# Performance work log

Measured on AMD Instinct MI355X. Metric: run time of the kernel, lower is better.

Reference implementation:

```python
import jax, jax.numpy as jnp
import numpy as np

N_PROBLEMS = 20000
N_SKILLS = 1000
EMB_SIZE = 128
TIME_LOG = 5.0
B, L = 64, 1024


def setup_inputs() -> dict:
    key = jax.random.key(0)
    ks = jax.random.split(key, 10)
    skills = jax.random.randint(ks[0], (B, L), 0, N_SKILLS)
    problems = jax.random.randint(ks[1], (B, L), 0, N_PROBLEMS)
    labels = jax.random.randint(ks[2], (B, L), 0, 2)
    times = jnp.sort(jax.random.randint(ks[3], (B, L), 0, 1_000_000), axis=-1)
    inp = jnp.stack([skills, problems, labels, times], axis=1)  # [B,4,L]
    std = 0.01
    return {
        "input": inp,
        "problem_base": std * jax.random.normal(ks[4], (N_PROBLEMS, 1), jnp.float32),
        "skill_base": std * jax.random.normal(ks[5], (N_SKILLS, 1), jnp.float32),
        "alpha_inter": std * jax.random.normal(ks[6], (N_SKILLS * 2, EMB_SIZE), jnp.float32),
        "alpha_skill": std * jax.random.normal(ks[7], (N_SKILLS, EMB_SIZE), jnp.float32),
        "beta_inter": std * jax.random.normal(ks[8], (N_SKILLS * 2, EMB_SIZE), jnp.float32),
        "beta_skill": std * jax.random.normal(ks[9], (N_SKILLS, EMB_SIZE), jnp.float32),
    }


def reference(input, problem_base, skill_base, alpha_inter, alpha_skill, beta_inter, beta_skill):
    skills = input[:, 0]    # [B,L]
    problems = input[:, 1]
    labels = input[:, 2]
    times = input[:, 3]

    mask_labels = labels * (labels < 2).astype(labels.dtype)
    inters = skills + mask_labels * N_SKILLS  # [B,L] in [0, 2*N_SKILLS)

    # pairwise Hawkes excitation / decay scores: [B,L,L]
    alphas = jnp.einsum('bie,bje->bij', alpha_inter[inters], alpha_skill[skills])
    betas = jnp.einsum('bie,bje->bij', beta_inter[inters], beta_skill[skills])
    betas = jnp.clip(betas + 1.0, 0.0, 10.0)

    dt = jnp.abs(times[:, :, None] - times[:, None, :]).astype(jnp.float32)
    log_dt = jnp.log(dt + 1e-10) / np.log(TIME_LOG)

    cross_effects = alphas * jnp.exp(-betas * log_dt)

    seq_len = skills.shape[1]
    # keep strictly-upper-triangular entries (source i before target j)
    keep = jnp.triu(jnp.ones((seq_len, seq_len), dtype=bool), k=1)
    sum_t = jnp.where(keep[None], cross_effects, 0.0).sum(axis=-2)  # [B,L]

    problem_bias = problem_base[problems][..., 0]
    skill_bias = skill_base[skills][..., 0]
    return jax.nn.sigmoid(problem_bias + skill_bias + sum_t)
```

## Files before the change

kernel.cpp:

```cpp
#include <hip/hip_runtime.h>
#include <hip/hip_bf16.h>

#define NB   64
#define SL   1024
#define EMB  128
#define NSK  1000
#define NS   4

#define AI_OFF 0
#define BI_OFF 256000
#define AS_OFF 512000
#define BS_OFF 640000
#define TB_ELEMS 768000
#define ACC_BYTE_OFF (TB_ELEMS * 2)

using short8  = __attribute__((ext_vector_type(8))) short;
using floatx4 = __attribute__((ext_vector_type(4))) float;

#define INV_LOG2_5 0.43067655807339306f

__device__ inline unsigned cvt2(float x, float y) {
    float2 f; f.x = x; f.y = y;
    __hip_bfloat162 h = __float22bfloat162_rn(f);
    unsigned u; __builtin_memcpy(&u, &h, sizeof(u));
    return u;
}

extern "C" __global__ __launch_bounds__(256)
void cvt_tables(const float* __restrict__ ai, const float* __restrict__ bi,
                const float* __restrict__ as, const float* __restrict__ bs,
                unsigned short* __restrict__ dst)
{
    const int t = blockIdx.x * 256 + threadIdx.x;
    const long e = (long)t * 8;
    const float* src;
    if      (e < 256000) src = ai + e;
    else if (e < 512000) src = bi + (e - 256000);
    else if (e < 640000) src = as + (e - 512000);
    else                 src = bs + (e - 640000);
    float4 f0 = *(const float4*)src;
    float4 f1 = *(const float4*)(src + 4);
    uint4 pk;
    pk.x = cvt2(f0.x, f0.y); pk.y = cvt2(f0.z, f0.w);
    pk.z = cvt2(f1.x, f1.y); pk.w = cvt2(f1.z, f1.w);
    *(uint4*)(dst + e) = pk;
}

__device__ float fixup_pair(const float* __restrict__ air,
                            const float* __restrict__ bir,
                            const float* __restrict__ asr,
                            const float* __restrict__ bsr) {
    float da = 0.f, db = 0.f;
    for (int k = 0; k < EMB; ++k) {
        da += air[k] * asr[k];
        db += bir[k] * bsr[k];
    }
    float beta = fminf(fmaxf(db + 1.f, 0.f), 10.f);
    return da * __expf(beta * 14.30676558073393f);
}

extern "C" __global__ __launch_bounds__(256, 2)
void hawkes_main(const int*   __restrict__ inp,
                 const unsigned short* __restrict__ tb,
                 float*       __restrict__ acc)
{
    __shared__ unsigned short lA[2][64][128];

    const int bid  = blockIdx.x;
    const int b    = bid & (NB - 1);
    const int r    = bid >> 6;
    const int jt   = 7 - (r >> 2);
    const int s    = r & 3;
    const int tid  = threadIdx.x;
    const int w    = tid >> 6;
    const int l    = tid & 63;
    const int quad = l >> 4;
    const int col  = l & 15;

    const int* __restrict__ binp = inp + b * 4 * SL;

    const int j0 = jt * 128 + w * 16 + col;
    const int j1 = j0 + 64;
    const int sk0 = binp[j0],          sk1 = binp[j1];
    const int tj0 = binp[3 * SL + j0], tj1 = binp[3 * SL + j1];

    short8 bfa0[4], bfb0[4], bfa1[4], bfb1[4];
    {
        const unsigned short* p0a = tb + AS_OFF + (long)sk0 * EMB + quad * 8;
        const unsigned short* p0b = tb + BS_OFF + (long)sk0 * EMB + quad * 8;
        const unsigned short* p1a = tb + AS_OFF + (long)sk1 * EMB + quad * 8;
        const unsigned short* p1b = tb + BS_OFF + (long)sk1 * EMB + quad * 8;
#pragma unroll
        for (int ks = 0; ks < 4; ++ks) {
            bfa0[ks] = *(const short8*)(p0a + ks * 32);
            bfb0[ks] = *(const short8*)(p0b + ks * 32);
            bfa1[ks] = *(const short8*)(p1a + ks * 32);
            bfb1[ks] = *(const short8*)(p1b + ks * 32);
        }
    }

    const int srow = tid >> 2;
    const int sq   = tid & 3;
    const int sw   = srow & 15;
    unsigned short* rowA = &lA[0][srow][0];
    unsigned short* rowB = &lA[1][srow][0];

    float sum0 = 0.f, sum1 = 0.f;
    const int itmax = 2 * jt + 1;

    if (s <= itmax) {
        uint4 pa0, pa1, pa2, pa3, pb0, pb1, pb2, pb3;
        {
            const int irow  = s * 64 + srow;
            const int ski   = binp[irow];
            const int li    = binp[2 * SL + irow];
            const long intr = ski + (long)li * NSK;
            const unsigned short* sA  = tb + AI_OFF + intr * EMB + sq * 32;
            const unsigned short* sBm = tb + BI_OFF + intr * EMB + sq * 32;
            pa0 = *(const uint4*)(sA);      pa1 = *(const uint4*)(sA + 8);
            pa2 = *(const uint4*)(sA + 16); pa3 = *(const uint4*)(sA + 24);
            pb0 = *(const uint4*)(sBm);     pb1 = *(const uint4*)(sBm + 8);
            pb2 = *(const uint4*)(sBm + 16);pb3 = *(const uint4*)(sBm + 24);
        }

        for (int it = s; it <= itmax; it += NS) {
            __syncthreads();
            *(uint4*)(rowA + (((sq * 4 + 0) ^ sw) * 8)) = pa0;
            *(uint4*)(rowA + (((sq * 4 + 1) ^ sw) * 8)) = pa1;
            *(uint4*)(rowA + (((sq * 4 + 2) ^ sw) * 8)) = pa2;
            *(uint4*)(rowA + (((sq * 4 + 3) ^ sw) * 8)) = pa3;
            *(uint4*)(rowB + (((sq * 4 + 0) ^ sw) * 8)) = pb0;
            *(uint4*)(rowB + (((sq * 4 + 1) ^ sw) * 8)) = pb1;
            *(uint4*)(rowB + (((sq * 4 + 2) ^ sw) * 8)) = pb2;
            *(uint4*)(rowB + (((sq * 4 + 3) ^ sw) * 8)) = pb3;

            if (it + NS <= itmax) {
                const int irow  = (it + NS) * 64 + srow;
                const int ski   = binp[irow];
                const int li    = binp[2 * SL + irow];
                const long intr = ski + (long)li * NSK;
                const unsigned short* sA  = tb + AI_OFF + intr * EMB + sq * 32;
                const unsigned short* sBm = tb + BI_OFF + intr * EMB + sq * 32;
                pa0 = *(const uint4*)(sA);      pa1 = *(const uint4*)(sA + 8);
                pa2 = *(const uint4*)(sA + 16); pa3 = *(const uint4*)(sA + 24);
                pb0 = *(const uint4*)(sBm);     pb1 = *(const uint4*)(sBm + 8);
                pb2 = *(const uint4*)(sBm + 16);pb3 = *(const uint4*)(sBm + 24);
            }
            __syncthreads();

            const int itb = it * 64;
#pragma unroll
            for (int isub = 0; isub < 4; ++isub) {
                floatx4 aa0 = {0.f,0.f,0.f,0.f}, bb0 = {0.f,0.f,0.f,0.f};
                floatx4 aa1 = {0.f,0.f,0.f,0.f}, bb1 = {0.f,0.f,0.f,0.f};
                const unsigned short* rrow0 = &lA[0][isub * 16 + col][0];
                const unsigned short* rrow1 = &lA[1][isub * 16 + col][0];
#pragma unroll
                for (int ks = 0; ks < 4; ++ks) {
                    const int pc = ((ks * 4 + quad) ^ col) * 8;
                    short8 av = *(const short8*)(rrow0 + pc);
                    short8 bv = *(const short8*)(rrow1 + pc);
                    aa0 = __builtin_amdgcn_mfma_f32_16x16x32_bf16(av, bfa0[ks], aa0, 0, 0, 0);
                    aa1 = __builtin_amdgcn_mfma_f32_16x16x32_bf16(av, bfa1[ks], aa1, 0, 0, 0);
                    bb0 = __builtin_amdgcn_mfma_f32_16x16x32_bf16(bv, bfb0[ks], bb0, 0, 0, 0);
                    bb1 = __builtin_amdgcn_mfma_f32_16x16x32_bf16(bv, bfb1[ks], bb1, 0, 0, 0);
                }
                const int ibase = itb + isub * 16 + quad * 4;
                const int4 t4 = *(const int4*)(binp + 3 * SL + ibase);
#pragma unroll
                for (int rr = 0; rr < 4; ++rr) {
                    const int ti = (rr == 0) ? t4.x : (rr == 1) ? t4.y : (rr == 2) ? t4.z : t4.w;
                    {
                        const int dt = tj0 - ti;
                        float lc  = __log2f((float)dt);
                        float nb  = fminf(fmaxf(bb0[rr] + 1.f, 0.f), 10.f) * (-INV_LOG2_5);
                        float arg = (dt > 0) ? nb * lc : -__builtin_inff();
                        sum0 += aa0[rr] * exp2f(arg);
                    }
                    {
                        const int dt = tj1 - ti;
                        float lc  = __log2f((float)dt);
                        float nb  = fminf(fmaxf(bb1[rr] + 1.f, 0.f), 10.f) * (-INV_LOG2_5);
                        float arg = (dt > 0) ? nb * lc : -__builtin_inff();
                        sum1 += aa1[rr] * exp2f(arg);
                    }
                }
            }
        }
    }

    sum0 += __shfl_xor(sum0, 16, 64); sum0 += __shfl_xor(sum0, 32, 64);
    sum1 += __shfl_xor(sum1, 16, 64); sum1 += __shfl_xor(sum1, 32, 64);

    if (quad == 0) {
        float* as_ = acc + (((long)s * NB + b) << 10);
        as_[j0] = sum0;
        as_[j1] = sum1;
    }
}

extern "C" __global__ __launch_bounds__(256)
void hawkes_finalize(const int* __restrict__ inp, const float* __restrict__ pbase,
                     const float* __restrict__ sbase,
                     const float* __restrict__ ai, const float* __restrict__ as,
                     const float* __restrict__ bi, const float* __restrict__ bs,
                     const float* __restrict__ acc, float* __restrict__ out)
{
    const int t = blockIdx.x * 256 + threadIdx.x;
    const int b = t >> 10, j = t & (SL - 1);
    const int* binp = inp + b * 4 * SL;
    const int tj   = binp[3 * SL + j];
    const int sk_j = binp[j];

    float corr = 0.f;
    for (int i = j - 1; i >= 0 && binp[3 * SL + i] == tj; --i) {
        const int ski = binp[i], li = binp[2 * SL + i];
        const long intr = ski + (long)li * NSK;
        corr += fixup_pair(ai + intr * EMB, bi + intr * EMB,
                           as + (long)sk_j * EMB, bs + (long)sk_j * EMB);
    }

    float sum = acc[t] + acc[NB * SL + t] + acc[2 * NB * SL + t] + acc[3 * NB * SL + t] + corr;
    const float x = pbase[binp[SL + j]] + sbase[sk_j] + sum;
    out[t] = 1.f / (1.f + __expf(-x));
}

extern "C" void kernel_launch(void* const* d_in, const int* in_sizes, int n_in,
                              void* d_out, int out_size, void* d_ws, size_t ws_size,
                              hipStream_t stream) {
    const int*   inp = (const int*)d_in[0];
    const float* pb  = (const float*)d_in[1];
    const float* sb  = (const float*)d_in[2];
    const float* ai  = (const float*)d_in[3];
    const float* as  = (const float*)d_in[4];
    const float* bi  = (const float*)d_in[5];
    const float* bs  = (const float*)d_in[6];

    unsigned short* tb  = (unsigned short*)d_ws;
    float*          acc = (float*)((char*)d_ws + ACC_BYTE_OFF);

    cvt_tables<<<dim3(96000 / 256), dim3(256), 0, stream>>>(ai, bi, as, bs, tb);
    hawkes_main<<<dim3(NB * 8 * NS), dim3(256), 0, stream>>>(inp, tb, acc);
    hawkes_finalize<<<dim3(NB * SL / 256), dim3(256), 0, stream>>>(
        inp, pb, sb, ai, as, bi, bs, acc, (float*)d_out);
}
```

Measured before the change: 118.4 us.

## Replace LDS-staged 256-thread blocks with single-wave blocks loading A fragments directly

The main kernel moves from 256-thread blocks that staged 64 source rows in shared memory (with two barriers per iteration) to one-wave blocks covering 32 target columns. Each block now reads the source-row A/B fragments straight from global memory into MFMA operands, with no LDS and no __syncthreads. The split count drops from 4 to 2, and finalize sums only two partial accumulators. Removing the barriers and giving finer causal load balance comes at the cost of losing reuse of each gathered source row across 4 waves, which roughly quadruples global and L2 gather traffic.

After: 158.1 us. 1.33x slower.

```diff
diff --git a/kernel.cpp b/kernel.cpp
--- a/kernel.cpp
+++ b/kernel.cpp
@@ -5,7 +5,7 @@
 #define SL   1024
 #define EMB  128
 #define NSK  1000
-#define NS   4
+#define NS   2
 
 #define AI_OFF 0
 #define BI_OFF 256000
@@ -59,28 +59,24 @@
     return da * __expf(beta * 14.30676558073393f);
 }
 
-extern "C" __global__ __launch_bounds__(256, 2)
+extern "C" __global__ __launch_bounds__(64, 3)
 void hawkes_main(const int*   __restrict__ inp,
                  const unsigned short* __restrict__ tb,
                  float*       __restrict__ acc)
 {
-    __shared__ unsigned short lA[2][64][128];
-
-    const int bid  = blockIdx.x;
-    const int b    = bid & (NB - 1);
-    const int r    = bid >> 6;
-    const int jt   = 7 - (r >> 2);
-    const int s    = r & 3;
-    const int tid  = threadIdx.x;
-    const int w    = tid >> 6;
-    const int l    = tid & 63;
+    const int u    = blockIdx.x;
+    const int jt   = 31 - (u >> 7);
+    const int rem  = u & 127;
+    const int b    = rem >> 1;
+    const int s    = rem & 1;
+    const int l    = threadIdx.x;
     const int quad = l >> 4;
     const int col  = l & 15;
 
     const int* __restrict__ binp = inp + b * 4 * SL;
 
-    const int j0 = jt * 128 + w * 16 + col;
-    const int j1 = j0 + 64;
+    const int j0 = jt * 32 + col;
+    const int j1 = j0 + 16;
     const int sk0 = binp[j0],          sk1 = binp[j1];
     const int tj0 = binp[3 * SL + j0], tj1 = binp[3 * SL + j1];
 
@@ -99,92 +95,48 @@
         }
     }
 
-    const int srow = tid >> 2;
-    const int sq   = tid & 3;
-    const int sw   = srow & 15;
-    unsigned short* rowA = &lA[0][srow][0];
-    unsigned short* rowB = &lA[1][srow][0];
+    float sum0 = 0.f, sum1 = 0.f;
+    const int kmax = 2 * jt + 1;
 
-    float sum0 = 0.f, sum1 = 0.f;
-    const int itmax = 2 * jt + 1;
+    for (int k = s; k <= kmax; k += NS) {
+        const int ibase = k * 16;
 
-    if (s <= itmax) {
-        uint4 pa0, pa1, pa2, pa3, pb0, pb1, pb2, pb3;
-        {
-            const int irow  = s * 64 + srow;
-            const int ski   = binp[irow];
-            const int li    = binp[2 * SL + irow];
-            const long intr = ski + (long)li * NSK;
-            const unsigned short* sA  = tb + AI_OFF + intr * EMB + sq * 32;
-            const unsigned short* sBm = tb + BI_OFF + intr * EMB + sq * 32;
-            pa0 = *(const uint4*)(sA);      pa1 = *(const uint4*)(sA + 8);
-            pa2 = *(const uint4*)(sA + 16); pa3 = *(const uint4*)(sA + 24);
-            pb0 = *(const uint4*)(sBm);     pb1 = *(const uint4*)(sBm + 8);
-            pb2 = *(const uint4*)(sBm + 16);pb3 = *(const uint4*)(sBm + 24);
+        const int ski   = binp[ibase + col];
+        const int li    = binp[2 * SL + ibase + col];
+        const long intr = ski + (long)li * NSK;
+        const unsigned short* rA = tb + AI_OFF + intr * EMB + quad * 8;
+        const unsigned short* rB = tb + BI_OFF + intr * EMB + quad * 8;
+
+        const int4 t4 = *(const int4*)(binp + 3 * SL + ibase + quad * 4);
+
+        floatx4 aa0 = {0.f,0.f,0.f,0.f}, bb0 = {0.f,0.f,0.f,0.f};
+        floatx4 aa1 = {0.f,0.f,0.f,0.f}, bb1 = {0.f,0.f,0.f,0.f};
+#pragma unroll
+        for (int ks = 0; ks < 4; ++ks) {
+            short8 av = *(const short8*)(rA + ks * 32);
+            short8 bv = *(const short8*)(rB + ks * 32);
+            aa0 = __builtin_amdgcn_mfma_f32_16x16x32_bf16(av, bfa0[ks], aa0, 0, 0, 0);
+            aa1 = __builtin_amdgcn_mfma_f32_16x16x32_bf16(av, bfa1[ks], aa1, 0, 0, 0);
+            bb0 = __builtin_amdgcn_mfma_f32_16x16x32_bf16(bv, bfb0[ks], bb0, 0, 0, 0);
+            bb1 = __builtin_amdgcn_mfma_f32_16x16x32_bf16(bv, bfb1[ks], bb1, 0, 0, 0);
         }
 
-        for (int it = s; it <= itmax; it += NS) {
-            __syncthreads();
-            *(uint4*)(rowA + (((sq * 4 + 0) ^ sw) * 8)) = pa0;
-            *(uint4*)(rowA + (((sq * 4 + 1) ^ sw) * 8)) = pa1;
-            *(uint4*)(rowA + (((sq * 4 + 2) ^ sw) * 8)) = pa2;
-            *(uint4*)(rowA + (((sq * 4 + 3) ^ sw) * 8)) = pa3;
-            *(uint4*)(rowB + (((sq * 4 + 0) ^ sw) * 8)) = pb0;
-            *(uint4*)(rowB + (((sq * 4 + 1) ^ sw) * 8)) = pb1;
-            *(uint4*)(rowB + (((sq * 4 + 2) ^ sw) * 8)) = pb2;
-            *(uint4*)(rowB + (((sq * 4 + 3) ^ sw) * 8)) = pb3;
-
-            if (it + NS <= itmax) {
-                const int irow  = (it + NS) * 64 + srow;
-                const int ski   = binp[irow];
-                const int li    = binp[2 * SL + irow];
-                const long intr = ski + (long)li * NSK;
-                const unsigned short* sA  = tb + AI_OFF + intr * EMB + sq * 32;
-                const unsigned short* sBm = tb + BI_OFF + intr * EMB + sq * 32;
-                pa0 = *(const uint4*)(sA);      pa1 = *(const uint4*)(sA + 8);
-                pa2 = *(const uint4*)(sA + 16); pa3 = *(const uint4*)(sA + 24);
-                pb0 = *(const uint4*)(sBm);     pb1 = *(const uint4*)(sBm + 8);
-                pb2 = *(const uint4*)(sBm + 16);pb3 = *(const uint4*)(sBm + 24);
+#pragma unroll
+        for (int rr = 0; rr < 4; ++rr) {
+            const int ti = (rr == 0) ? t4.x : (rr == 1) ? t4.y : (rr == 2) ? t4.z : t4.w;
+            {
+                const int dt = tj0 - ti;
+                float lc   = __log2f((float)dt) * (-INV_LOG2_5);
+                float beta = fminf(fmaxf(bb0[rr] + 1.f, 0.f), 10.f);
+                float arg  = (dt > 0) ? beta * lc : -__builtin_inff();
+                sum0 += aa0[rr] * exp2f(arg);
             }
-            __syncthreads();
-
-            const int itb = it * 64;
-#pragma unroll
-            for (int isub = 0; isub < 4; ++isub) {
-                floatx4 aa0 = {0.f,0.f,0.f,0.f}, bb0 = {0.f,0.f,0.f,0.f};
-                floatx4 aa1 = {0.f,0.f,0.f,0.f}, bb1 = {0.f,0.f,0.f,0.f};
-                const unsigned short* rrow0 = &lA[0][isub * 16 + col][0];
-                const unsigned short* rrow1 = &lA[1][isub * 16 + col][0];
-#pragma unroll
-                for (int ks = 0; ks < 4; ++ks) {
-                    const int pc = ((ks * 4 + quad) ^ col) * 8;
-                    short8 av = *(const short8*)(rrow0 + pc);
-                    short8 bv = *(const short8*)(rrow1 + pc);
-                    aa0 = __builtin_amdgcn_mfma_f32_16x16x32_bf16(av, bfa0[ks], aa0, 0, 0, 0);
-                    aa1 = __builtin_amdgcn_mfma_f32_16x16x32_bf16(av, bfa1[ks], aa1, 0, 0, 0);
-                    bb0 = __builtin_amdgcn_mfma_f32_16x16x32_bf16(bv, bfb0[ks], bb0, 0, 0, 0);
-                    bb1 = __builtin_amdgcn_mfma_f32_16x16x32_bf16(bv, bfb1[ks], bb1, 0, 0, 0);
-                }
-                const int ibase = itb + isub * 16 + quad * 4;
-                const int4 t4 = *(const int4*)(binp + 3 * SL + ibase);
-#pragma unroll
-                for (int rr = 0; rr < 4; ++rr) {
-                    const int ti = (rr == 0) ? t4.x : (rr == 1) ? t4.y : (rr == 2) ? t4.z : t4.w;
-                    {
-                        const int dt = tj0 - ti;
-                        float lc  = __log2f((float)dt);
-                        float nb  = fminf(fmaxf(bb0[rr] + 1.f, 0.f), 10.f) * (-INV_LOG2_5);
-                        float arg = (dt > 0) ? nb * lc : -__builtin_inff();
-                        sum0 += aa0[rr] * exp2f(arg);
-                    }
-                    {
-                        const int dt = tj1 - ti;
-                        float lc  = __log2f((float)dt);
-                        float nb  = fminf(fmaxf(bb1[rr] + 1.f, 0.f), 10.f) * (-INV_LOG2_5);
-                        float arg = (dt > 0) ? nb * lc : -__builtin_inff();
-                        sum1 += aa1[rr] * exp2f(arg);
-                    }
-                }
+            {
+                const int dt = tj1 - ti;
+                float lc   = __log2f((float)dt) * (-INV_LOG2_5);
+                float beta = fminf(fmaxf(bb1[rr] + 1.f, 0.f), 10.f);
+                float arg  = (dt > 0) ? beta * lc : -__builtin_inff();
+                sum1 += aa1[rr] * exp2f(arg);
             }
         }
     }
@@ -220,7 +172,7 @@
                            as + (long)sk_j * EMB, bs + (long)sk_j * EMB);
     }
 
-    float sum = acc[t] + acc[NB * SL + t] + acc[2 * NB * SL + t] + acc[3 * NB * SL + t] + corr;
+    float sum = acc[t] + acc[NB * SL + t] + corr;
     const float x = pbase[binp[SL + j]] + sbase[sk_j] + sum;
     out[t] = 1.f / (1.f + __expf(-x));
 }
@@ -240,7 +192,7 @@
     float*          acc = (float*)((char*)d_ws + ACC_BYTE_OFF);
 
     cvt_tables<<<dim3(96000 / 256), dim3(256), 0, stream>>>(ai, bi, as, bs, tb);
-    hawkes_main<<<dim3(NB * 8 * NS), dim3(256), 0, stream>>>(inp, tb, acc);
+    hawkes_main<<<dim3(NB * 32 * NS), dim3(64), 0, stream>>>(inp, tb, acc);
     hawkes_finalize<<<dim3(NB * SL / 256), dim3(256), 0, stream>>>(
         inp, pb, sb, ai, as, bi, bs, acc, (float*)d_out);
 }
```
